# Performance work log

Hardware: AMD Instinct MI355X
Metric: run time of the kernel (lower is better)

Reference implementation:

```python
import jax, jax.numpy as jnp
import numpy as np

B, N, D, H = 1, 4096, 512, 8
HD = D // H


def setup_inputs() -> dict:
    key = jax.random.key(0)
    ks = jax.random.split(key, 12)
    s = 0.02  # weight init scale for numerical stability
    query = jax.random.normal(ks[0], (B, N, D), jnp.float32)
    key_t = jax.random.normal(ks[1], (B, N, D), jnp.float32)
    value = jax.random.normal(ks[2], (B, N, D), jnp.float32)
    Wq = jax.random.normal(ks[3], (D, D), jnp.float32) * s
    bq = jax.random.normal(ks[4], (D,), jnp.float32) * s
    Wk = jax.random.normal(ks[5], (D, D), jnp.float32) * s
    bk = jax.random.normal(ks[6], (D,), jnp.float32) * s
    Wv = jax.random.normal(ks[7], (D, D), jnp.float32) * s
    bv = jax.random.normal(ks[8], (D,), jnp.float32) * s
    Wo = jax.random.normal(ks[9], (D, D), jnp.float32) * s
    bo = jax.random.normal(ks[10], (D,), jnp.float32) * s
    # build sgconv_mat exactly as __init__: shifted nonneg adjacency, max-normalized,
    # then symmetric degree normalization D^-1/2 A D^-1/2 (gwmha_layer_num=1)
    A = jax.random.uniform(ks[11], (N, N), jnp.float32)
    A = A + A.min()
    A = A / A.max()
    deg = A.sum(1)
    dinv = 1.0 / jnp.sqrt(deg)
    sgconv_mat = (dinv[:, None] * A * dinv[None, :])[None]  # [1,N,N]
    return {"query": query, "key": key_t, "value": value,
            "Wq": Wq, "bq": bq, "Wk": Wk, "bk": bk, "Wv": Wv, "bv": bv,
            "Wo": Wo, "bo": bo, "sgconv_mat": sgconv_mat}


def reference(query, key, value, Wq, bq, Wk, bk, Wv, bv, Wo, bo, sgconv_mat):
    b, n, d = query.shape
    q = (query @ Wq.T + bq).reshape(b, n, H, HD)
    k = (key @ Wk.T + bk).reshape(b, n, H, HD)
    v = (value @ Wv.T + bv).reshape(b, n, H, HD)
    energy = jnp.einsum('bqhd,bkhd->bhqk', q, k)
    attn = jax.nn.softmax(energy / jnp.sqrt(jnp.float32(d)), axis=3)
    out = jnp.einsum('bhqk,bkhd->bqhd', attn, v).reshape(b, n, d)
    out = sgconv_mat @ out          # [1,N,N] @ [B,N,D] -> [B,N,D]
    return out @ Wo.T + bo
```

## Files before the change

### kernel.cpp

```cpp
#include <hip/hip_runtime.h>
#include <hip/hip_bf16.h>
#include <math.h>

typedef __bf16 bf16_t;
typedef __bf16 bf16x8 __attribute__((ext_vector_type(8)));
typedef float floatx4 __attribute__((ext_vector_type(4)));

typedef __attribute__((address_space(1))) void gvoid_t;
typedef __attribute__((address_space(3))) void lvoid_t;

static __device__ __forceinline__ void gload_lds16(const bf16_t* g, const bf16_t* l) {
    __builtin_amdgcn_global_load_lds((gvoid_t*)(size_t)g,
                                     (lvoid_t*)(unsigned)(size_t)l,
                                     16, 0, 0);
}

static __device__ __forceinline__ unsigned pack_bf2(float lo, float hi) {
    bf16_t a = (bf16_t)lo, b = (bf16_t)hi;
    return (unsigned)__builtin_bit_cast(unsigned short, a)
         | ((unsigned)__builtin_bit_cast(unsigned short, b) << 16);
}

static __device__ inline void store_c(float* C, size_t i, float v) { C[i] = v; }
static __device__ inline void store_c(bf16_t* C, size_t i, float v) { C[i] = (bf16_t)v; }

static __device__ inline void cvt8(const float* src, bf16_t* dst, size_t idx) {
    float4 a = *(const float4*)(src + idx);
    float4 c = *(const float4*)(src + idx + 4);
    uint4 u;
    u.x = pack_bf2(a.x, a.y);
    u.y = pack_bf2(a.z, a.w);
    u.z = pack_bf2(c.x, c.y);
    u.w = pack_bf2(c.z, c.w);
    *(uint4*)(dst + idx) = u;
}

template <typename TC>
__device__ inline void gemm_body128(
    const bf16_t* __restrict__ A, int lda,
    const bf16_t* __restrict__ B, int ldb,
    const float* __restrict__ bias_col, const float* __restrict__ bias_row,
    float cscale,
    TC* __restrict__ C, int ldc, int K, int m0, int n0)
{
    __shared__ bf16_t As[128 * 32];
    __shared__ bf16_t Bs[128 * 32];

    const int tid = threadIdx.x;
    const int lane = tid & 63, wave = tid >> 6;
    const int wm = wave & 1, wn = wave >> 1;
    const int lo16 = lane & 15, quad = lane >> 4;

    const int r0 = tid >> 2;
    const int s0 = tid & 3;
    const int c0 = s0 ^ ((r0 >> 1) & 3);
    const bf16_t* ga0 = A + (size_t)(m0 + r0) * lda + c0 * 8;
    const bf16_t* ga1 = A + (size_t)(m0 + 64 + r0) * lda + c0 * 8;
    const bf16_t* gb0 = B + (size_t)(n0 + r0) * ldb + c0 * 8;
    const bf16_t* gb1 = B + (size_t)(n0 + 64 + r0) * ldb + c0 * 8;
    const bf16_t* la0 = As + wave * 512;
    const bf16_t* la1 = As + 2048 + wave * 512;
    const bf16_t* lb0 = Bs + wave * 512;
    const bf16_t* lb1 = Bs + 2048 + wave * 512;

    int aoff[4], boff[4];
#pragma unroll
    for (int t = 0; t < 4; ++t) {
        const int ra = wm * 64 + t * 16 + lo16;
        aoff[t] = ra * 32 + ((quad ^ ((ra >> 1) & 3)) << 3);
        const int rb = wn * 64 + t * 16 + lo16;
        boff[t] = rb * 32 + ((quad ^ ((rb >> 1) & 3)) << 3);
    }

    floatx4 acc[4][4] = {};

    for (int k0 = 0; k0 < K; k0 += 32) {
        __syncthreads();
        gload_lds16(ga0 + k0, la0);
        gload_lds16(ga1 + k0, la1);
        gload_lds16(gb0 + k0, lb0);
        gload_lds16(gb1 + k0, lb1);
        __syncthreads();

        bf16x8 af[4], bfv[4];
#pragma unroll
        for (int t = 0; t < 4; ++t) {
            af[t]  = *(const bf16x8*)(As + aoff[t]);
            bfv[t] = *(const bf16x8*)(Bs + boff[t]);
        }
#pragma unroll
        for (int mt = 0; mt < 4; ++mt)
#pragma unroll
            for (int nt = 0; nt < 4; ++nt)
                acc[mt][nt] = __builtin_amdgcn_mfma_f32_16x16x32_bf16(
                    af[mt], bfv[nt], acc[mt][nt], 0, 0, 0);
    }

#pragma unroll
    for (int nt = 0; nt < 4; ++nt) {
        const int gn = n0 + wn * 64 + nt * 16 + lo16;
        const float bc = bias_col ? bias_col[gn] : 0.f;
#pragma unroll
        for (int mt = 0; mt < 4; ++mt) {
#pragma unroll
            for (int r = 0; r < 4; ++r) {
                const int gm = m0 + wm * 64 + mt * 16 + quad * 4 + r;
                float v = acc[mt][nt][r] + bc;
                if (bias_row) v += bias_row[gm];
                store_c(C, (size_t)gm * ldc + gn, v * cscale);
            }
        }
    }
}

__global__ __launch_bounds__(256) void prep(
    const float* __restrict__ query, const float* __restrict__ key, const float* __restrict__ value,
    const float* __restrict__ Wq, const float* __restrict__ Wk,
    const float* __restrict__ Wv, const float* __restrict__ Wo,
    bf16_t* qB, bf16_t* kB, bf16_t* vB,
    bf16_t* wqB, bf16_t* wkB, bf16_t* wvB, bf16_t* woB)
{
    const int b = blockIdx.x;
    const float* src; bf16_t* dst; size_t base;
    if      (b < 256) { src = query; dst = qB;  base = (size_t)b * 8192; }
    else if (b < 512) { src = key;   dst = kB;  base = (size_t)(b - 256) * 8192; }
    else if (b < 768) { src = value; dst = vB;  base = (size_t)(b - 512) * 8192; }
    else if (b < 800) { src = Wq;    dst = wqB; base = (size_t)(b - 768) * 8192; }
    else if (b < 832) { src = Wk;    dst = wkB; base = (size_t)(b - 800) * 8192; }
    else if (b < 864) { src = Wv;    dst = wvB; base = (size_t)(b - 832) * 8192; }
    else              { src = Wo;    dst = woB; base = (size_t)(b - 864) * 8192; }
#pragma unroll
    for (int it = 0; it < 4; ++it)
        cvt8(src, dst, base + (size_t)it * 2048 + threadIdx.x * 8);
}

__global__ __launch_bounds__(256) void proj_qkv(
    const bf16_t* __restrict__ qB, const bf16_t* __restrict__ wqB, const float* __restrict__ bq,
    const bf16_t* __restrict__ kB, const bf16_t* __restrict__ wkB, const float* __restrict__ bk,
    const bf16_t* __restrict__ wvB, const bf16_t* __restrict__ vB, const float* __restrict__ bv,
    bf16_t* __restrict__ q, bf16_t* __restrict__ k, bf16_t* __restrict__ vt, float qscale)
{
    const int b = blockIdx.x;
    const int i = b & 127;
    if (b < 256) {
        const int m0 = (i & 31) * 128, n0 = (i >> 5) * 128;
        if (b < 128)
            gemm_body128<bf16_t>(qB, 512, wqB, 512, bq, nullptr, qscale, q, 512, 512, m0, n0);
        else
            gemm_body128<bf16_t>(kB, 512, wkB, 512, bk, nullptr, 1.f, k, 512, 512, m0, n0);
    } else {
        const int m0 = (i & 3) * 128, n0 = (i >> 2) * 128;
        gemm_body128<bf16_t>(wvB, 512, vB, 512, nullptr, bv, 1.f, vt, 4096, 512, m0, n0);
    }
}

__global__ __launch_bounds__(256) void sgconv_gemm(
    const bf16_t* __restrict__ sgb, const bf16_t* __restrict__ aot,
    float* __restrict__ part)
{
    const int i = blockIdx.x & 127;
    const int kb = blockIdx.x >> 7;
    const int m0 = (i & 31) * 128, n0 = (i >> 5) * 128;
    const int kbase = kb * 1024;
    gemm_body128<float>(sgb + kbase, 4096, aot + kbase, 4096, nullptr, nullptr, 1.f,
                        part + (size_t)kb * (4096 * 512), 512, 1024, m0, n0);
}

__global__ __launch_bounds__(256) void part_reduce(
    const float* __restrict__ p, bf16_t* __restrict__ o2)
{
    const size_t S = (size_t)4096 * 512;
    const size_t idx = ((size_t)blockIdx.x * 256 + threadIdx.x) * 8;
    uint4 u;
#pragma unroll
    for (int half = 0; half < 2; ++half) {
        float4 s = *(const float4*)(p + idx + half * 4);
#pragma unroll
        for (int kb = 1; kb < 4; ++kb) {
            float4 t = *(const float4*)(p + kb * S + idx + half * 4);
            s.x += t.x; s.y += t.y; s.z += t.z; s.w += t.w;
        }
        if (half == 0) { u.x = pack_bf2(s.x, s.y); u.y = pack_bf2(s.z, s.w); }
        else           { u.z = pack_bf2(s.x, s.y); u.w = pack_bf2(s.z, s.w); }
    }
    *(uint4*)(o2 + idx) = u;
}

__global__ __launch_bounds__(256) void out_proj(
    const bf16_t* __restrict__ o2, const bf16_t* __restrict__ woB,
    const float* __restrict__ bo, float* __restrict__ out)
{
    const int i = blockIdx.x, x = i & 7, t = i >> 3;
    const int n0 = (t & 7) * 64;
    const int m0 = ((t >> 3) * 8 + x) * 64;

    __shared__ bf16_t As[64 * 68];
    __shared__ bf16_t Bs[64 * 68];

    const int tid = threadIdx.x;
    const int lane = tid & 63, wave = tid >> 6;
    const int wm = wave & 1, wn = wave >> 1;
    const int lo16 = lane & 15, quad = lane >> 4;
    const int sr = tid >> 2, sc = (tid & 3) * 8;

    floatx4 acc[2][2] = {};

    for (int k0 = 0; k0 < 512; k0 += 32) {
        bf16x8 a0 = *(const bf16x8*)(o2 + (size_t)(m0 + sr) * 512 + k0 + sc);
        bf16x8 b0 = *(const bf16x8*)(woB + (size_t)(n0 + sr) * 512 + k0 + sc);
        __syncthreads();
        *(bf16x8*)(&As[sr * 68 + sc]) = a0;
        *(bf16x8*)(&Bs[sr * 68 + sc]) = b0;
        __syncthreads();

        bf16x8 af[2], bfv[2];
#pragma unroll
        for (int mt = 0; mt < 2; ++mt)
            af[mt] = *(const bf16x8*)(&As[(wm * 32 + mt * 16 + lo16) * 68 + quad * 8]);
#pragma unroll
        for (int nt = 0; nt < 2; ++nt)
            bfv[nt] = *(const bf16x8*)(&Bs[(wn * 32 + nt * 16 + lo16) * 68 + quad * 8]);
#pragma unroll
        for (int mt = 0; mt < 2; ++mt)
#pragma unroll
            for (int nt = 0; nt < 2; ++nt)
                acc[mt][nt] = __builtin_amdgcn_mfma_f32_16x16x32_bf16(
                    af[mt], bfv[nt], acc[mt][nt], 0, 0, 0);
    }

#pragma unroll
    for (int nt = 0; nt < 2; ++nt) {
        const int gn = n0 + wn * 32 + nt * 16 + lo16;
        const float bc = bo[gn];
#pragma unroll
        for (int mt = 0; mt < 2; ++mt)
#pragma unroll
            for (int r = 0; r < 4; ++r) {
                const int gm = m0 + wm * 32 + mt * 16 + quad * 4 + r;
                out[(size_t)gm * 512 + gn] = acc[mt][nt][r] + bc;
            }
    }
}

__global__ __launch_bounds__(256, 4) void flash_attn(
    const bf16_t* __restrict__ q, const bf16_t* __restrict__ kk,
    const bf16_t* __restrict__ vt, float* __restrict__ op,
    float* __restrict__ lp,
    const float* __restrict__ sg, bf16_t* __restrict__ sgb)
{
    const unsigned bid = blockIdx.x;
    const unsigned rm = bid % 3u;
    if (rm) {
        const size_t base = (size_t)((bid / 3u) * 2u + (rm - 1u)) * 8192;
#pragma unroll
        for (int it = 0; it < 4; ++it)
            cvt8(sg, sgb, base + (size_t)it * 2048 + threadIdx.x * 8);
        return;
    }
    const int fid = bid / 3u;

    const int N = 4096, D = 512;
    const int h   = fid & 7;
    const int qb  = (fid >> 3) & 31;
    const int qtr = fid >> 8;
    const int t0  = qtr * 1024;

    const int tid = threadIdx.x;
    const int w = tid >> 6, lane = tid & 63;
    const int lo16 = lane & 15, quad = lane >> 4;

    __shared__ bf16_t Ks[64 * 72];
    __shared__ bf16_t Vs[64 * 72];
    __shared__ bf16_t Ps[4][32 * 72];

    const bf16_t* qp = q + (size_t)(qb * 128 + w * 32 + lo16) * D + h * 64 + quad * 8;
    bf16x8 qf[2][2];
    qf[0][0] = *(const bf16x8*)qp;
    qf[0][1] = *(const bf16x8*)(qp + 32);
    qf[1][0] = *(const bf16x8*)(qp + 16 * D);
    qf[1][1] = *(const bf16x8*)(qp + 16 * D + 32);

    const int srow = tid >> 2, sc = (tid & 3) * 16;
    const bf16_t* ksrc = kk + (size_t)(t0 + srow) * D + h * 64 + sc;
    const bf16_t* vsrc = vt + (size_t)(h * 64 + srow) * N + t0 + sc;
    bf16_t* kdst = &Ks[srow * 72 + sc];
    bf16_t* vdst = &Vs[srow * 72 + sc];

    floatx4 o[4][2] = {};
    float l[2] = {0.f, 0.f};

    bf16x8 kr0 = *(const bf16x8*)ksrc;
    bf16x8 kr1 = *(const bf16x8*)(ksrc + 8);
    bf16x8 vr0 = *(const bf16x8*)vsrc;
    bf16x8 vr1 = *(const bf16x8*)(vsrc + 8);

    for (int it = 0; it < 16; ++it) {
        __syncthreads();
        *(bf16x8*)kdst = kr0;  *(bf16x8*)(kdst + 8) = kr1;
        *(bf16x8*)vdst = vr0;  *(bf16x8*)(vdst + 8) = vr1;
        __syncthreads();
        if (it < 15) {
            const bf16_t* kn = ksrc + (size_t)(it + 1) * 64 * D;
            const bf16_t* vn = vsrc + (it + 1) * 64;
            kr0 = *(const bf16x8*)kn;  kr1 = *(const bf16x8*)(kn + 8);
            vr0 = *(const bf16x8*)vn;  vr1 = *(const bf16x8*)(vn + 8);
        }

        floatx4 s[4][2];
#pragma unroll
        for (int tt = 0; tt < 4; ++tt) {
            bf16x8 kf0 = *(const bf16x8*)(&Ks[(tt * 16 + lo16) * 72 + quad * 8]);
            bf16x8 kf1 = *(const bf16x8*)(&Ks[(tt * 16 + lo16) * 72 + 32 + quad * 8]);
#pragma unroll
            for (int qt = 0; qt < 2; ++qt) {
                floatx4 a = {};
                a = __builtin_amdgcn_mfma_f32_16x16x32_bf16(kf0, qf[qt][0], a, 0, 0, 0);
                a = __builtin_amdgcn_mfma_f32_16x16x32_bf16(kf1, qf[qt][1], a, 0, 0, 0);
                s[tt][qt] = a;
            }
        }
#pragma unroll
        for (int tt = 0; tt < 4; ++tt)
#pragma unroll
            for (int qt = 0; qt < 2; ++qt) {
                float e0 = exp2f(s[tt][qt][0]);
                float e1 = exp2f(s[tt][qt][1]);
                float e2 = exp2f(s[tt][qt][2]);
                float e3 = exp2f(s[tt][qt][3]);
                l[qt] += (e0 + e1) + (e2 + e3);
                uint2 pk;
                pk.x = pack_bf2(e0, e1);
                pk.y = pack_bf2(e2, e3);
                *(uint2*)(&Ps[w][(qt * 16 + lo16) * 72 + tt * 16 + quad * 4]) = pk;
            }
#pragma unroll
        for (int ks = 0; ks < 2; ++ks) {
            bf16x8 pf0 = *(const bf16x8*)(&Ps[w][lo16 * 72 + ks * 32 + quad * 8]);
            bf16x8 pf1 = *(const bf16x8*)(&Ps[w][(16 + lo16) * 72 + ks * 32 + quad * 8]);
#pragma unroll
            for (int t = 0; t < 4; ++t) {
                bf16x8 vf = *(const bf16x8*)(&Vs[(t * 16 + lo16) * 72 + ks * 32 + quad * 8]);
                o[t][0] = __builtin_amdgcn_mfma_f32_16x16x32_bf16(vf, pf0, o[t][0], 0, 0, 0);
                o[t][1] = __builtin_amdgcn_mfma_f32_16x16x32_bf16(vf, pf1, o[t][1], 0, 0, 0);
            }
        }
    }

#pragma unroll
    for (int qt = 0; qt < 2; ++qt) {
        l[qt] += __shfl_xor(l[qt], 16);
        l[qt] += __shfl_xor(l[qt], 32);
    }

    const int g = fid & 255;
    float* opw = op + ((size_t)qtr * 256 + g) * 8192;
#pragma unroll
    for (int t = 0; t < 4; ++t)
#pragma unroll
        for (int pt = 0; pt < 2; ++pt)
#pragma unroll
            for (int r = 0; r < 4; ++r)
                opw[(t * 16 + quad * 4 + r) * 128 + w * 32 + pt * 16 + lo16] = o[t][pt][r];

    if (quad == 0) {
        float* lpw = lp + ((size_t)qtr * 256 + g) * 128;
        lpw[w * 32 + lo16] = l[0];
        lpw[w * 32 + 16 + lo16] = l[1];
    }
}

__global__ __launch_bounds__(256) void attn_combine(
    const float* __restrict__ op, const float* __restrict__ lp, bf16_t* __restrict__ aot)
{
    const int g = blockIdx.x;
    const int h = g & 7, qb = g >> 3;
    const int tid = threadIdx.x;
    __shared__ float ls[128];
    if (tid < 128) {
        float s = 0.f;
#pragma unroll
        for (int qtr = 0; qtr < 4; ++qtr)
            s += lp[((size_t)qtr * 256 + g) * 128 + tid];
        ls[tid] = 1.0f / s;
    }
    __syncthreads();
    const float* b0 = op + (size_t)g * 8192;
    const size_t QS = (size_t)256 * 8192;
#pragma unroll 4
    for (int i = 0; i < 32; ++i) {
        int idx = i * 256 + tid;
        float v = b0[idx] + b0[QS + idx] + b0[2 * QS + idx] + b0[3 * QS + idx];
        int dim = idx >> 7, qc = idx & 127;
        aot[(size_t)(h * 64 + dim) * 4096 + qb * 128 + qc] = (bf16_t)(v * ls[qc]);
    }
}

extern "C" void kernel_launch(void* const* d_in, const int* in_sizes, int n_in,
                              void* d_out, int out_size, void* d_ws, size_t ws_size,
                              hipStream_t stream)
{
    const int N = 4096, D = 512;
    const float* query = (const float*)d_in[0];
    const float* key_t = (const float*)d_in[1];
    const float* value = (const float*)d_in[2];
    const float* Wq = (const float*)d_in[3];
    const float* bq = (const float*)d_in[4];
    const float* Wk = (const float*)d_in[5];
    const float* bk = (const float*)d_in[6];
    const float* Wv = (const float*)d_in[7];
    const float* bv = (const float*)d_in[8];
    const float* Wo = (const float*)d_in[9];
    const float* bo = (const float*)d_in[10];
    const float* sg = (const float*)d_in[11];
    float* out = (float*)d_out;

    const size_t ND = (size_t)N * D;
    const size_t DD = (size_t)D * D;

    char* base = (char*)d_ws;
    bf16_t* q    = (bf16_t*)base;
    bf16_t* kk   = q   + ND;
    bf16_t* vt   = kk  + ND;
    bf16_t* aot  = vt  + ND;
    bf16_t* sgb  = aot + ND;
    char* regA   = (char*)(sgb + (size_t)N * N);
    bf16_t* qB   = (bf16_t*)regA;
    bf16_t* kB   = qB + ND;
    bf16_t* vB   = kB + ND;
    bf16_t* wqB  = vB + ND;
    bf16_t* wkB  = wqB + DD;
    bf16_t* wvB  = wkB + DD;
    float* op    = (float*)regA;
    float* p     = (float*)regA;
    char* tail   = regA + (size_t)4 * 256 * 8192 * 4;
    float*  lp   = (float*)tail;
    bf16_t* woB  = (bf16_t*)(lp + (size_t)4 * 256 * 128);
    bf16_t* o2   = woB + DD;

    const dim3 blk(256);

    prep<<<896, blk, 0, stream>>>(query, key_t, value, Wq, Wk, Wv, Wo,
                                  qB, kB, vB, wqB, wkB, wvB, woB);

    const float qscale = 1.44269504088896f / sqrtf((float)D);
    proj_qkv<<<384, blk, 0, stream>>>(qB, wqB, bq, kB, wkB, bk,
                                      wvB, vB, bv, q, kk, vt, qscale);

    flash_attn<<<3072, blk, 0, stream>>>(q, kk, vt, op, lp, sg, sgb);
    attn_combine<<<256, blk, 0, stream>>>(op, lp, aot);

    sgconv_gemm<<<512, blk, 0, stream>>>(sgb, aot, p);
    part_reduce<<<1024, blk, 0, stream>>>(p, o2);
    out_proj<<<512, blk, 0, stream>>>(o2, woB, bo, out);

    (void)in_sizes; (void)n_in; (void)out_size; (void)ws_size;
}
```

Baseline: 278.5 us.

## Move sgconv conversion into projection kernel and compute row sums via MFMA

The fp32-to-bf16 conversion of the sgconv matrix moves out of the flash attention launch and into extra blocks of the projection kernel, so the attention grid holds only attention blocks. Softmax row sums are now built with an MFMA against a ones vector on the bf16 probabilities, replacing the per-lane adds and cross-lane shuffles. exp2f becomes the hardware exp2 intrinsic. The MFMA row sum uses bf16-rounded probabilities, which changes the normaliser slightly, and it adds two MFMAs per k-step.

```diff
diff --git a/kernel.cpp b/kernel.cpp
--- a/kernel.cpp
+++ b/kernel.cpp
@@ -138,9 +138,17 @@
     const bf16_t* __restrict__ qB, const bf16_t* __restrict__ wqB, const float* __restrict__ bq,
     const bf16_t* __restrict__ kB, const bf16_t* __restrict__ wkB, const float* __restrict__ bk,
     const bf16_t* __restrict__ wvB, const bf16_t* __restrict__ vB, const float* __restrict__ bv,
-    bf16_t* __restrict__ q, bf16_t* __restrict__ k, bf16_t* __restrict__ vt, float qscale)
+    bf16_t* __restrict__ q, bf16_t* __restrict__ k, bf16_t* __restrict__ vt, float qscale,
+    const float* __restrict__ sg, bf16_t* __restrict__ sgb)
 {
     const int b = blockIdx.x;
+    if (b >= 384) {
+        const size_t base = (size_t)(b - 384) * 8192;
+#pragma unroll
+        for (int it = 0; it < 4; ++it)
+            cvt8(sg, sgb, base + (size_t)it * 2048 + threadIdx.x * 8);
+        return;
+    }
     const int i = b & 127;
     if (b < 256) {
         const int m0 = (i & 31) * 128, n0 = (i >> 5) * 128;
@@ -245,19 +253,9 @@
 __global__ __launch_bounds__(256, 4) void flash_attn(
     const bf16_t* __restrict__ q, const bf16_t* __restrict__ kk,
     const bf16_t* __restrict__ vt, float* __restrict__ op,
-    float* __restrict__ lp,
-    const float* __restrict__ sg, bf16_t* __restrict__ sgb)
-{
-    const unsigned bid = blockIdx.x;
-    const unsigned rm = bid % 3u;
-    if (rm) {
-        const size_t base = (size_t)((bid / 3u) * 2u + (rm - 1u)) * 8192;
-#pragma unroll
-        for (int it = 0; it < 4; ++it)
-            cvt8(sg, sgb, base + (size_t)it * 2048 + threadIdx.x * 8);
-        return;
-    }
-    const int fid = bid / 3u;
+    float* __restrict__ lp)
+{
+    const int fid = blockIdx.x;
 
     const int N = 4096, D = 512;
     const int h   = fid & 7;
@@ -286,8 +284,12 @@
     bf16_t* kdst = &Ks[srow * 72 + sc];
     bf16_t* vdst = &Vs[srow * 72 + sc];
 
+    bf16x8 ones;
+#pragma unroll
+    for (int i = 0; i < 8; ++i) ones[i] = (bf16_t)1.0f;
+
     floatx4 o[4][2] = {};
-    float l[2] = {0.f, 0.f};
+    floatx4 lacc[2] = {};
 
     bf16x8 kr0 = *(const bf16x8*)ksrc;
     bf16x8 kr1 = *(const bf16x8*)(ksrc + 8);
@@ -323,11 +325,10 @@
         for (int tt = 0; tt < 4; ++tt)
 #pragma unroll
             for (int qt = 0; qt < 2; ++qt) {
-                float e0 = exp2f(s[tt][qt][0]);
-                float e1 = exp2f(s[tt][qt][1]);
-                float e2 = exp2f(s[tt][qt][2]);
-                float e3 = exp2f(s[tt][qt][3]);
-                l[qt] += (e0 + e1) + (e2 + e3);
+                float e0 = __builtin_amdgcn_exp2f(s[tt][qt][0]);
+                float e1 = __builtin_amdgcn_exp2f(s[tt][qt][1]);
+                float e2 = __builtin_amdgcn_exp2f(s[tt][qt][2]);
+                float e3 = __builtin_amdgcn_exp2f(s[tt][qt][3]);
                 uint2 pk;
                 pk.x = pack_bf2(e0, e1);
                 pk.y = pack_bf2(e2, e3);
@@ -337,6 +338,8 @@
         for (int ks = 0; ks < 2; ++ks) {
             bf16x8 pf0 = *(const bf16x8*)(&Ps[w][lo16 * 72 + ks * 32 + quad * 8]);
             bf16x8 pf1 = *(const bf16x8*)(&Ps[w][(16 + lo16) * 72 + ks * 32 + quad * 8]);
+            lacc[0] = __builtin_amdgcn_mfma_f32_16x16x32_bf16(ones, pf0, lacc[0], 0, 0, 0);
+            lacc[1] = __builtin_amdgcn_mfma_f32_16x16x32_bf16(ones, pf1, lacc[1], 0, 0, 0);
 #pragma unroll
             for (int t = 0; t < 4; ++t) {
                 bf16x8 vf = *(const bf16x8*)(&Vs[(t * 16 + lo16) * 72 + ks * 32 + quad * 8]);
@@ -346,12 +349,6 @@
         }
     }
 
-#pragma unroll
-    for (int qt = 0; qt < 2; ++qt) {
-        l[qt] += __shfl_xor(l[qt], 16);
-        l[qt] += __shfl_xor(l[qt], 32);
-    }
-
     const int g = fid & 255;
     float* opw = op + ((size_t)qtr * 256 + g) * 8192;
 #pragma unroll
@@ -364,8 +361,8 @@
 
     if (quad == 0) {
         float* lpw = lp + ((size_t)qtr * 256 + g) * 128;
-        lpw[w * 32 + lo16] = l[0];
-        lpw[w * 32 + 16 + lo16] = l[1];
+        lpw[w * 32 + lo16] = lacc[0][0];
+        lpw[w * 32 + 16 + lo16] = lacc[1][0];
     }
 }
 
@@ -443,10 +440,10 @@
                                   qB, kB, vB, wqB, wkB, wvB, woB);
 
     const float qscale = 1.44269504088896f / sqrtf((float)D);
-    proj_qkv<<<384, blk, 0, stream>>>(qB, wqB, bq, kB, wkB, bk,
-                                      wvB, vB, bv, q, kk, vt, qscale);
-
-    flash_attn<<<3072, blk, 0, stream>>>(q, kk, vt, op, lp, sg, sgb);
+    proj_qkv<<<2432, blk, 0, stream>>>(qB, wqB, bq, kB, wkB, bk,
+                                       wvB, vB, bv, q, kk, vt, qscale, sg, sgb);
+
+    flash_attn<<<1024, blk, 0, stream>>>(q, kk, vt, op, lp);
     attn_combine<<<256, blk, 0, stream>>>(op, lp, aot);
 
     sgconv_gemm<<<512, blk, 0, stream>>>(sgb, aot, p);
```

New measurement: 257.1 us. 1.08x faster.
